# Performance work log

Measured on AMD Instinct MI355X. Metric: run time of the kernel, lower is better.

Reference implementation:

```python
import jax, jax.numpy as jnp
import numpy as np

N_NODES = 50000
N_EDGES = 1_000_000
D_IN = 64
HID = 64
N_GRAPHS = 128


def setup_inputs() -> dict:
    key = jax.random.key(0)
    ks = jax.random.split(key, 12)
    s = 1.0 / np.sqrt(HID)
    x = jax.random.normal(ks[0], (N_NODES, D_IN), dtype=jnp.float32)
    edge_index = jax.random.randint(ks[1], (2, N_EDGES), 0, N_NODES, dtype=jnp.int32)
    # every graph id occupied, sorted (like PyG batch vector)
    batch_index = (jnp.arange(N_NODES, dtype=jnp.int32) * N_GRAPHS) // N_NODES
    return {
        "x": x,
        "Wl0": jax.random.normal(ks[2], (HID, D_IN), jnp.float32) * s,
        "Wr0": jax.random.normal(ks[3], (HID, D_IN), jnp.float32) * s,
        "bl0": jax.random.normal(ks[4], (HID,), jnp.float32) * s,
        "Wl": jax.random.normal(ks[5], (HID, HID), jnp.float32) * s,
        "Wr": jax.random.normal(ks[6], (HID, HID), jnp.float32) * s,
        "bl": jax.random.normal(ks[7], (HID,), jnp.float32) * s,
        "W1": jax.random.normal(ks[8], (HID, HID), jnp.float32) * s,
        "b1": jax.random.normal(ks[9], (HID,), jnp.float32) * s,
        "W2": jax.random.normal(ks[10], (3, HID), jnp.float32) * s,
        "b2": jax.random.normal(ks[11], (3,), jnp.float32) * s,
        "edge_index": edge_index,
        "batch_index": batch_index,
    }


def _sage_conv(x, Wl, Wr, bl, src, dst, n_nodes):
    # PyG SAGEConv (aggr='mean'): out = lin_l(mean_{j in N(i)} x_j) + lin_r(x_i)
    msgs = jnp.take(x, src, axis=0)                               # [E, D] gather
    agg = jax.ops.segment_sum(msgs, dst, num_segments=n_nodes)    # [N, D] scatter-add
    deg = jax.ops.segment_sum(jnp.ones((src.shape[0],), x.dtype), dst, num_segments=n_nodes)
    mean = agg / jnp.clip(deg, 1.0)[:, None]
    return mean @ Wl.T + bl + x @ Wr.T


def reference(x, Wl0, Wr0, bl0, Wl, Wr, bl, W1, b1, W2, b2, edge_index, batch_index):
    src, dst = edge_index[0], edge_index[1]
    n = x.shape[0]
    h = jnp.tanh(_sage_conv(x, Wl0, Wr0, bl0, src, dst, n))
    # same SAGEConv instance reused 3 times
    for _ in range(3):
        h = jnp.tanh(_sage_conv(h, Wl, Wr, bl, src, dst, n))
    pooled = jax.ops.segment_max(h, batch_index, num_segments=N_GRAPHS)  # [G, H]
    # same lin1 reused 3 times
    g = pooled
    for _ in range(3):
        g = jnp.tanh(g @ W1.T + b1)
    return g @ W2.T + b2
```

## Files before the change

kernel.cpp:

```cpp
#include <hip/hip_runtime.h>
#include <math.h>

#define NT 256

typedef unsigned short ushort_t;
typedef unsigned int uint_t;

__device__ __forceinline__ float rlf(float v, int l) {
    return __int_as_float(__builtin_amdgcn_readlane(__float_as_int(v), l));
}
__device__ __forceinline__ int rli(int v, int l) {
    return __builtin_amdgcn_readlane(v, l);
}
__device__ __forceinline__ int imax(int a, int b) { return a > b ? a : b; }

__device__ __forceinline__ ushort_t f2bf_rne(float f) {
    uint_t u = __float_as_uint(f);
    uint_t r = u + 0x7FFF + ((u >> 16) & 1);
    return (ushort_t)(r >> 16);
}
__device__ __forceinline__ float bf2f(ushort_t b) {
    return __uint_as_float(((uint_t)b) << 16);
}


__global__ void zero_i32(int* __restrict__ p, int n) {
    int t = blockIdx.x * blockDim.x + threadIdx.x;
    if (t < n) p[t] = 0;
}

__global__ void hist_dst(int* __restrict__ cnt, const int* __restrict__ dst, int n_edges) {
    int e = blockIdx.x * blockDim.x + threadIdx.x;
    if (e < n_edges) atomicAdd(&cnt[dst[e]], 1);
}

__global__ void scan_blocks(const int* __restrict__ cnt, int* __restrict__ bsum, int n) {
    __shared__ int s[NT];
    int i = blockIdx.x * NT + threadIdx.x;
    s[threadIdx.x] = (i < n) ? cnt[i] : 0;
    __syncthreads();
    for (int off = NT / 2; off > 0; off >>= 1) {
        if (threadIdx.x < off) s[threadIdx.x] += s[threadIdx.x + off];
        __syncthreads();
    }
    if (threadIdx.x == 0) bsum[blockIdx.x] = s[0];
}

__global__ void scan_bsum(const int* __restrict__ bsum, int* __restrict__ boff,
                          int nb, int* __restrict__ row_off, int n) {
    __shared__ int s[1024];
    int tid = threadIdx.x;
    int v = (tid < nb) ? bsum[tid] : 0;
    s[tid] = v;
    __syncthreads();
    for (int off = 1; off < 1024; off <<= 1) {
        int t = (tid >= off) ? s[tid - off] : 0;
        __syncthreads();
        s[tid] += t;
        __syncthreads();
    }
    if (tid < nb) boff[tid] = s[tid] - v;
    if (tid == nb - 1) row_off[n] = s[tid];
}

__global__ void scan_final(const int* __restrict__ cnt, const int* __restrict__ boff,
                           int* __restrict__ row_off, int* __restrict__ cursor, int n) {
    __shared__ int s[NT];
    int i = blockIdx.x * NT + threadIdx.x;
    int v = (i < n) ? cnt[i] : 0;
    s[threadIdx.x] = v;
    __syncthreads();
    for (int off = 1; off < NT; off <<= 1) {
        int t = (threadIdx.x >= off) ? s[threadIdx.x - off] : 0;
        __syncthreads();
        s[threadIdx.x] += t;
        __syncthreads();
    }
    if (i < n) {
        int ex = boff[blockIdx.x] + s[threadIdx.x] - v;
        row_off[i] = ex;
        cursor[i] = ex;
    }
}

__global__ void edge_scatter(int* __restrict__ csr_src, int* __restrict__ cursor,
                             const int* __restrict__ src, const int* __restrict__ dst,
                             int n_edges) {
    int e = blockIdx.x * blockDim.x + threadIdx.x;
    if (e < n_edges) {
        int p = atomicAdd(&cursor[dst[e]], 1);
        csr_src[p] = src[e];
    }
}

__global__ void wtrans(float* __restrict__ out, const float* __restrict__ W) {
    int t = blockIdx.x * blockDim.x + threadIdx.x;
    if (t < 4096) {
        int kk = t & 3, f = (t >> 2) & 63, k4 = t >> 8;
        out[t] = W[f * 64 + k4 * 4 + kk];
    }
}

__global__ void f2bf_kern(ushort_t* __restrict__ o, const float* __restrict__ in, int n) {
    int t = blockIdx.x * blockDim.x + threadIdx.x;
    if (t < n) o[t] = f2bf_rne(in[t]);
}


__global__ void pool_init(float* __restrict__ pooled, int n) {
    int t = blockIdx.x * blockDim.x + threadIdx.x;
    if (t < n) pooled[t] = -INFINITY;
}

__device__ __forceinline__ void atomicMaxFloat(float* addr, float value) {
    if (value >= 0.0f)
        atomicMax((int*)addr, __float_as_int(value));
    else
        atomicMin((unsigned int*)addr, (unsigned int)__float_as_int(value));
}

__global__ __launch_bounds__(NT, 8) void sage_layer(
    float* __restrict__ out, ushort_t* __restrict__ out_bf,
    float* __restrict__ pooled,
    const float* __restrict__ h_in, const ushort_t* __restrict__ hb_in,
    const int* __restrict__ row_off, const int* __restrict__ csr_src,
    const int* __restrict__ batch,
    const float* __restrict__ Wl, const float* __restrict__ WrT,
    const float* __restrict__ bl,
    int n_nodes, int do_pool) {
    __shared__ float WL[4096];
    int tid = threadIdx.x;
    for (int t = tid; t < 4096; t += NT) {
        int kk = t & 3, f = (t >> 2) & 63, k4 = t >> 8;
        WL[t] = Wl[f * 64 + k4 * 4 + kk];
    }
    __syncthreads();

    int lane = tid & 63;
    int gwave = (blockIdx.x * NT + tid) >> 6;
    int nwaves = (gridDim.x * NT) >> 6;
    float bias = bl[lane];

    for (int q = gwave; q * 4 < n_nodes; q += nwaves) {
        int base = q * 4;
        float mean0 = 0.f, mean1 = 0.f, mean2 = 0.f, mean3 = 0.f;
        float hv0 = 0.f, hv1 = 0.f, hv2 = 0.f, hv3 = 0.f;

#define GATHER_NODE(MEAN, HV, N)                                              \
        {                                                                     \
            int i = base + (N);                                               \
            if (i < n_nodes) {                                                \
                int beg = row_off[i];                                         \
                int end_ = row_off[i + 1];                                    \
                int deg = end_ - beg;                                         \
                float a0 = 0.f, a1 = 0.f;                                     \
                for (int cb = beg; cb < end_; cb += 64) {                     \
                    int m = end_ - cb; if (m > 64) m = 64;                    \
                    int lidx = cb + (lane < m ? lane : m - 1);                \
                    int idx = csr_src[lidx];                                  \
                    for (int j = 0; j < m; j += 8) {                          \
                        int mm1 = m - 1;                                      \
                        int s0 = rli(idx, j);                                 \
                        int s1 = rli(idx, j + 1 < m ? j + 1 : mm1);           \
                        int s2 = rli(idx, j + 2 < m ? j + 2 : mm1);           \
                        int s3 = rli(idx, j + 3 < m ? j + 3 : mm1);           \
                        int s4 = rli(idx, j + 4 < m ? j + 4 : mm1);           \
                        int s5 = rli(idx, j + 5 < m ? j + 5 : mm1);           \
                        int s6 = rli(idx, j + 6 < m ? j + 6 : mm1);           \
                        int s7 = rli(idx, j + 7 < m ? j + 7 : mm1);           \
                        float v0 = bf2f(hb_in[(s0 << 6) + lane]);             \
                        float v1 = bf2f(hb_in[(s1 << 6) + lane]);             \
                        float v2 = bf2f(hb_in[(s2 << 6) + lane]);             \
                        float v3 = bf2f(hb_in[(s3 << 6) + lane]);             \
                        float v4 = bf2f(hb_in[(s4 << 6) + lane]);             \
                        float v5 = bf2f(hb_in[(s5 << 6) + lane]);             \
                        float v6 = bf2f(hb_in[(s6 << 6) + lane]);             \
                        float v7 = bf2f(hb_in[(s7 << 6) + lane]);             \
                        a0 += v0;                                             \
                        a1 += (j + 1 < m) ? v1 : 0.f;                         \
                        a0 += (j + 2 < m) ? v2 : 0.f;                         \
                        a1 += (j + 3 < m) ? v3 : 0.f;                         \
                        a0 += (j + 4 < m) ? v4 : 0.f;                         \
                        a1 += (j + 5 < m) ? v5 : 0.f;                         \
                        a0 += (j + 6 < m) ? v6 : 0.f;                         \
                        a1 += (j + 7 < m) ? v7 : 0.f;                         \
                    }                                                         \
                }                                                             \
                MEAN = (a0 + a1) * (1.0f / (float)(deg > 0 ? deg : 1));       \
                HV = h_in[(size_t)i * 64 + lane];                             \
            }                                                                 \
        }

        GATHER_NODE(mean0, hv0, 0)
        GATHER_NODE(mean1, hv1, 1)
        GATHER_NODE(mean2, hv2, 2)
        GATHER_NODE(mean3, hv3, 3)
#undef GATHER_NODE

        float o0 = bias, o1 = bias, o2 = bias, o3 = bias;
        for (int k4 = 0; k4 < 16; ++k4) {
            float4 wl = *(const float4*)&WL[k4 * 256 + lane * 4];
            float4 wr = *(const float4*)&WrT[k4 * 256 + lane * 4];
            int kb = k4 * 4;
#define DENSE_KK(WLK, WRK, KK)                                                \
            {                                                                 \
                int k = kb + (KK);                                            \
                o0 += rlf(mean0, k) * (WLK) + rlf(hv0, k) * (WRK);            \
                o1 += rlf(mean1, k) * (WLK) + rlf(hv1, k) * (WRK);            \
                o2 += rlf(mean2, k) * (WLK) + rlf(hv2, k) * (WRK);            \
                o3 += rlf(mean3, k) * (WLK) + rlf(hv3, k) * (WRK);            \
            }
            DENSE_KK(wl.x, wr.x, 0)
            DENSE_KK(wl.y, wr.y, 1)
            DENSE_KK(wl.z, wr.z, 2)
            DENSE_KK(wl.w, wr.w, 3)
#undef DENSE_KK
        }

        o0 = tanhf(o0); o1 = tanhf(o1); o2 = tanhf(o2); o3 = tanhf(o3);

#define WRITE_NODE(O, N)                                                      \
        {                                                                     \
            int i = base + (N);                                               \
            if (i < n_nodes) {                                                \
                if (do_pool) {                                                \
                    atomicMaxFloat(&pooled[(size_t)batch[i] * 64 + lane], O); \
                } else {                                                      \
                    out[(size_t)i * 64 + lane] = O;                           \
                    out_bf[(size_t)i * 64 + lane] = f2bf_rne(O);              \
                }                                                             \
            }                                                                 \
        }
        WRITE_NODE(o0, 0)
        WRITE_NODE(o1, 1)
        WRITE_NODE(o2, 2)
        WRITE_NODE(o3, 3)
#undef WRITE_NODE
    }
}

__global__ void head(float* __restrict__ out, const float* __restrict__ pooled,
                     const float* __restrict__ W1, const float* __restrict__ b1,
                     const float* __restrict__ W2, const float* __restrict__ b2) {
    __shared__ float W1T[64][64];
    int tid = threadIdx.x;
    for (int t = tid; t < 4096; t += NT) {
        int f = t >> 6, k = t & 63;
        W1T[k][f] = W1[t];
    }
    __syncthreads();

    int lane = tid & 63;
    int g = blockIdx.x * (NT >> 6) + (tid >> 6);
    float v = pooled[(size_t)g * 64 + lane];
    float bias = b1[lane];
#pragma unroll
    for (int it = 0; it < 3; ++it) {
        float acc = bias;
#pragma unroll
        for (int k = 0; k < 64; ++k) {
            acc += rlf(v, k) * W1T[k][lane];
        }
        v = tanhf(acc);
    }
#pragma unroll
    for (int j = 0; j < 3; ++j) {
        float p = v * W2[j * 64 + lane];
#pragma unroll
        for (int off = 32; off >= 1; off >>= 1) p += __shfl_xor(p, off);
        if (lane == 0) out[g * 3 + j] = p + b2[j];
    }
}


extern "C" void kernel_launch(void* const* d_in, const int* in_sizes, int n_in,
                              void* d_out, int out_size, void* d_ws, size_t ws_size,
                              hipStream_t stream) {
    const float* x   = (const float*)d_in[0];
    const float* Wl0 = (const float*)d_in[1];
    const float* Wr0 = (const float*)d_in[2];
    const float* bl0 = (const float*)d_in[3];
    const float* Wl  = (const float*)d_in[4];
    const float* Wr  = (const float*)d_in[5];
    const float* bl  = (const float*)d_in[6];
    const float* W1  = (const float*)d_in[7];
    const float* b1  = (const float*)d_in[8];
    const float* W2  = (const float*)d_in[9];
    const float* b2  = (const float*)d_in[10];
    const int* ei    = (const int*)d_in[11];
    const int* batch = (const int*)d_in[12];

    int n_nodes = in_sizes[0] / 64;
    int n_edges = in_sizes[11] / 2;
    const int* src = ei;
    const int* dst = ei + n_edges;

    int nb = (n_nodes + NT - 1) / NT;
    size_t nfeat = (size_t)n_nodes * 64;

    float* bufA   = (float*)d_ws;
    float* bufB   = bufA + nfeat;
    int* csr_src  = (int*)(bufB + nfeat);
    int* row_off  = csr_src + n_edges;
    int* cursor   = row_off + (n_nodes + 1);
    int* cnt      = cursor + n_nodes;
    int* bsum     = cnt + n_nodes;
    int* boff     = bsum + nb;
    float* pooled = (float*)(boff + nb);
    float* wr0t   = pooled + 128 * 64;
    float* wrt    = wr0t + 4096;
    ushort_t* bfA = (ushort_t*)(wrt + 4096);
    ushort_t* bfB = bfA + nfeat;

    int eblk = (n_edges + NT - 1) / NT;
    const int pers_blk = 2048;

    zero_i32<<<nb, NT, 0, stream>>>(cnt, n_nodes);
    hist_dst<<<eblk, NT, 0, stream>>>(cnt, dst, n_edges);
    scan_blocks<<<nb, NT, 0, stream>>>(cnt, bsum, n_nodes);
    scan_bsum<<<1, 1024, 0, stream>>>(bsum, boff, nb, row_off, n_nodes);
    scan_final<<<nb, NT, 0, stream>>>(cnt, boff, row_off, cursor, n_nodes);
    edge_scatter<<<eblk, NT, 0, stream>>>(csr_src, cursor, src, dst, n_edges);

    wtrans<<<16, NT, 0, stream>>>(wr0t, Wr0);
    wtrans<<<16, NT, 0, stream>>>(wrt, Wr);
    f2bf_kern<<<(int)((nfeat + NT - 1) / NT), NT, 0, stream>>>(bfA, x, (int)nfeat);
    pool_init<<<(128 * 64 + NT - 1) / NT, NT, 0, stream>>>(pooled, 128 * 64);

    sage_layer<<<pers_blk, NT, 0, stream>>>(bufA, bfB, pooled, x, bfA,
                                            row_off, csr_src, batch,
                                            Wl0, wr0t, bl0, n_nodes, 0);
    sage_layer<<<pers_blk, NT, 0, stream>>>(bufB, bfA, pooled, bufA, bfB,
                                            row_off, csr_src, batch,
                                            Wl, wrt, bl, n_nodes, 0);
    sage_layer<<<pers_blk, NT, 0, stream>>>(bufA, bfB, pooled, bufB, bfA,
                                            row_off, csr_src, batch,
                                            Wl, wrt, bl, n_nodes, 0);
    sage_layer<<<pers_blk, NT, 0, stream>>>(bufB, bfA, pooled, bufA, bfB,
                                            row_off, csr_src, batch,
                                            Wl, wrt, bl, n_nodes, 1);

    head<<<32, NT, 0, stream>>>((float*)d_out, pooled, W1, b1, W2, b2);
}
```

Measured before the change: 458.9 us.

## Compute SAGE dense transform with bf16 MFMA over shared-memory node tiles

```diff
diff --git a/kernel.cpp b/kernel.cpp
--- a/kernel.cpp
+++ b/kernel.cpp
@@ -5,10 +5,9 @@
 
 typedef unsigned short ushort_t;
 typedef unsigned int uint_t;
-
-__device__ __forceinline__ float rlf(float v, int l) {
-    return __int_as_float(__builtin_amdgcn_readlane(__float_as_int(v), l));
-}
+typedef __attribute__((ext_vector_type(8))) short bf16x8;
+typedef __attribute__((ext_vector_type(4))) float f32x4;
+
 __device__ __forceinline__ int rli(int v, int l) {
     return __builtin_amdgcn_readlane(v, l);
 }
@@ -21,6 +20,9 @@
 }
 __device__ __forceinline__ float bf2f(ushort_t b) {
     return __uint_as_float(((uint_t)b) << 16);
+}
+__device__ __forceinline__ float rlf(float v, int l) {
+    return __int_as_float(__builtin_amdgcn_readlane(__float_as_int(v), l));
 }
 
 
@@ -93,17 +95,25 @@
     }
 }
 
-__global__ void wtrans(float* __restrict__ out, const float* __restrict__ W) {
-    int t = blockIdx.x * blockDim.x + threadIdx.x;
-    if (t < 4096) {
-        int kk = t & 3, f = (t >> 2) & 63, k4 = t >> 8;
-        out[t] = W[f * 64 + k4 * 4 + kk];
-    }
-}
 
 __global__ void f2bf_kern(ushort_t* __restrict__ o, const float* __restrict__ in, int n) {
     int t = blockIdx.x * blockDim.x + threadIdx.x;
     if (t < n) o[t] = f2bf_rne(in[t]);
+}
+
+__global__ void pack_w(ushort_t* __restrict__ packed, const float* __restrict__ Wl,
+                       const float* __restrict__ Wr) {
+    int t = blockIdx.x * blockDim.x + threadIdx.x;
+    if (t < 8192) {
+        int i = t & 7;
+        int lane = (t >> 3) & 63;
+        int nt = (t >> 9) & 3;
+        int ks = t >> 11;
+        int k = ks * 32 + ((lane >> 4) << 3) + i;
+        int f = nt * 16 + (lane & 15);
+        float w = (k < 64) ? Wl[f * 64 + k] : Wr[f * 64 + (k - 64)];
+        packed[t] = f2bf_rne(w);
+    }
 }
 
 
@@ -120,122 +130,111 @@
 }
 
 __global__ __launch_bounds__(NT, 8) void sage_layer(
-    float* __restrict__ out, ushort_t* __restrict__ out_bf,
-    float* __restrict__ pooled,
-    const float* __restrict__ h_in, const ushort_t* __restrict__ hb_in,
+    ushort_t* __restrict__ out_bf, float* __restrict__ pooled,
+    const ushort_t* __restrict__ hb_in,
     const int* __restrict__ row_off, const int* __restrict__ csr_src,
     const int* __restrict__ batch,
-    const float* __restrict__ Wl, const float* __restrict__ WrT,
+    const ushort_t* __restrict__ pw,
     const float* __restrict__ bl,
     int n_nodes, int do_pool) {
-    __shared__ float WL[4096];
+    __shared__ ushort_t A[32 * 136];
     int tid = threadIdx.x;
-    for (int t = tid; t < 4096; t += NT) {
-        int kk = t & 3, f = (t >> 2) & 63, k4 = t >> 8;
-        WL[t] = Wl[f * 64 + k4 * 4 + kk];
-    }
-    __syncthreads();
-
     int lane = tid & 63;
-    int gwave = (blockIdx.x * NT + tid) >> 6;
-    int nwaves = (gridDim.x * NT) >> 6;
-    float bias = bl[lane];
-
-    for (int q = gwave; q * 4 < n_nodes; q += nwaves) {
-        int base = q * 4;
-        float mean0 = 0.f, mean1 = 0.f, mean2 = 0.f, mean3 = 0.f;
-        float hv0 = 0.f, hv1 = 0.f, hv2 = 0.f, hv3 = 0.f;
-
-#define GATHER_NODE(MEAN, HV, N)                                              \
-        {                                                                     \
-            int i = base + (N);                                               \
-            if (i < n_nodes) {                                                \
-                int beg = row_off[i];                                         \
-                int end_ = row_off[i + 1];                                    \
-                int deg = end_ - beg;                                         \
-                float a0 = 0.f, a1 = 0.f;                                     \
-                for (int cb = beg; cb < end_; cb += 64) {                     \
-                    int m = end_ - cb; if (m > 64) m = 64;                    \
-                    int lidx = cb + (lane < m ? lane : m - 1);                \
-                    int idx = csr_src[lidx];                                  \
-                    for (int j = 0; j < m; j += 8) {                          \
-                        int mm1 = m - 1;                                      \
-                        int s0 = rli(idx, j);                                 \
-                        int s1 = rli(idx, j + 1 < m ? j + 1 : mm1);           \
-                        int s2 = rli(idx, j + 2 < m ? j + 2 : mm1);           \
-                        int s3 = rli(idx, j + 3 < m ? j + 3 : mm1);           \
-                        int s4 = rli(idx, j + 4 < m ? j + 4 : mm1);           \
-                        int s5 = rli(idx, j + 5 < m ? j + 5 : mm1);           \
-                        int s6 = rli(idx, j + 6 < m ? j + 6 : mm1);           \
-                        int s7 = rli(idx, j + 7 < m ? j + 7 : mm1);           \
-                        float v0 = bf2f(hb_in[(s0 << 6) + lane]);             \
-                        float v1 = bf2f(hb_in[(s1 << 6) + lane]);             \
-                        float v2 = bf2f(hb_in[(s2 << 6) + lane]);             \
-                        float v3 = bf2f(hb_in[(s3 << 6) + lane]);             \
-                        float v4 = bf2f(hb_in[(s4 << 6) + lane]);             \
-                        float v5 = bf2f(hb_in[(s5 << 6) + lane]);             \
-                        float v6 = bf2f(hb_in[(s6 << 6) + lane]);             \
-                        float v7 = bf2f(hb_in[(s7 << 6) + lane]);             \
-                        a0 += v0;                                             \
-                        a1 += (j + 1 < m) ? v1 : 0.f;                         \
-                        a0 += (j + 2 < m) ? v2 : 0.f;                         \
-                        a1 += (j + 3 < m) ? v3 : 0.f;                         \
-                        a0 += (j + 4 < m) ? v4 : 0.f;                         \
-                        a1 += (j + 5 < m) ? v5 : 0.f;                         \
-                        a0 += (j + 6 < m) ? v6 : 0.f;                         \
-                        a1 += (j + 7 < m) ? v7 : 0.f;                         \
-                    }                                                         \
-                }                                                             \
-                MEAN = (a0 + a1) * (1.0f / (float)(deg > 0 ? deg : 1));       \
-                HV = h_in[(size_t)i * 64 + lane];                             \
-            }                                                                 \
+    int v = tid >> 6;
+    int g0 = blockIdx.x * 32 + v * 8;
+
+    int roidx = g0 + (lane < 9 ? lane : 8);
+    if (roidx > n_nodes) roidx = n_nodes;
+    int ro = row_off[roidx];
+
+#pragma unroll
+    for (int n = 0; n < 8; ++n) {
+        int g = g0 + n;
+        int row = v * 8 + n;
+        if (g < n_nodes) {
+            int b = rli(ro, n);
+            int e_ = rli(ro, n + 1);
+            int d = e_ - b;
+            float mean = 0.f;
+            if (d <= 64) {
+                int idx = csr_src[b + (lane < d ? lane : imax(d - 1, 0))];
+                float a0 = 0.f, a1 = 0.f;
+                for (int j = 0; j < d; j += 8) {
+                    int mm1 = d - 1;
+                    int s0 = rli(idx, j);
+                    int s1 = rli(idx, j + 1 < d ? j + 1 : mm1);
+                    int s2 = rli(idx, j + 2 < d ? j + 2 : mm1);
+                    int s3 = rli(idx, j + 3 < d ? j + 3 : mm1);
+                    int s4 = rli(idx, j + 4 < d ? j + 4 : mm1);
+                    int s5 = rli(idx, j + 5 < d ? j + 5 : mm1);
+                    int s6 = rli(idx, j + 6 < d ? j + 6 : mm1);
+                    int s7 = rli(idx, j + 7 < d ? j + 7 : mm1);
+                    float v0 = bf2f(hb_in[(s0 << 6) + lane]);
+                    float v1 = bf2f(hb_in[(s1 << 6) + lane]);
+                    float v2 = bf2f(hb_in[(s2 << 6) + lane]);
+                    float v3 = bf2f(hb_in[(s3 << 6) + lane]);
+                    float v4 = bf2f(hb_in[(s4 << 6) + lane]);
+                    float v5 = bf2f(hb_in[(s5 << 6) + lane]);
+                    float v6 = bf2f(hb_in[(s6 << 6) + lane]);
+                    float v7 = bf2f(hb_in[(s7 << 6) + lane]);
+                    a0 += v0;
+                    a1 += (j + 1 < d) ? v1 : 0.f;
+                    a0 += (j + 2 < d) ? v2 : 0.f;
+                    a1 += (j + 3 < d) ? v3 : 0.f;
+                    a0 += (j + 4 < d) ? v4 : 0.f;
+                    a1 += (j + 5 < d) ? v5 : 0.f;
+                    a0 += (j + 6 < d) ? v6 : 0.f;
+                    a1 += (j + 7 < d) ? v7 : 0.f;
+                }
+                mean = (a0 + a1) * (1.0f / (float)imax(d, 1));
+            } else {
+                float aa = 0.f;
+                for (int cb = b; cb < e_; cb += 64) {
+                    int m = e_ - cb; if (m > 64) m = 64;
+                    int lidx = cb + (lane < m ? lane : m - 1);
+                    int idx = csr_src[lidx];
+                    for (int j = 0; j < m; ++j)
+                        aa += bf2f(hb_in[(rli(idx, j) << 6) + lane]);
+                }
+                mean = aa * (1.0f / (float)imax(d, 1));
+            }
+            A[row * 136 + lane] = f2bf_rne(mean);
+            A[row * 136 + 64 + lane] = hb_in[(size_t)g * 64 + lane];
+        } else {
+            A[row * 136 + lane] = 0;
+            A[row * 136 + 64 + lane] = 0;
         }
-
-        GATHER_NODE(mean0, hv0, 0)
-        GATHER_NODE(mean1, hv1, 1)
-        GATHER_NODE(mean2, hv2, 2)
-        GATHER_NODE(mean3, hv3, 3)
-#undef GATHER_NODE
-
-        float o0 = bias, o1 = bias, o2 = bias, o3 = bias;
-        for (int k4 = 0; k4 < 16; ++k4) {
-            float4 wl = *(const float4*)&WL[k4 * 256 + lane * 4];
-            float4 wr = *(const float4*)&WrT[k4 * 256 + lane * 4];
-            int kb = k4 * 4;
-#define DENSE_KK(WLK, WRK, KK)                                                \
-            {                                                                 \
-                int k = kb + (KK);                                            \
-                o0 += rlf(mean0, k) * (WLK) + rlf(hv0, k) * (WRK);            \
-                o1 += rlf(mean1, k) * (WLK) + rlf(hv1, k) * (WRK);            \
-                o2 += rlf(mean2, k) * (WLK) + rlf(hv2, k) * (WRK);            \
-                o3 += rlf(mean3, k) * (WLK) + rlf(hv3, k) * (WRK);            \
+    }
+    __syncthreads();
+
+    int rowtile = v >> 1;
+    int a_row = rowtile * 16 + (lane & 15);
+    int kbase = (lane >> 4) << 3;
+#pragma unroll
+    for (int p = 0; p < 2; ++p) {
+        int nt = (v & 1) * 2 + p;
+        f32x4 acc = {0.f, 0.f, 0.f, 0.f};
+#pragma unroll
+        for (int ks = 0; ks < 4; ++ks) {
+            bf16x8 af = *reinterpret_cast<const bf16x8*>(&A[a_row * 136 + ks * 32 + kbase]);
+            bf16x8 bf = *reinterpret_cast<const bf16x8*>(&pw[(((ks << 2) + nt) * 64 + lane) << 3]);
+            acc = __builtin_amdgcn_mfma_f32_16x16x32_bf16(af, bf, acc, 0, 0, 0);
+        }
+        int c = nt * 16 + (lane & 15);
+        float bias = bl[c];
+        int rbase = blockIdx.x * 32 + rowtile * 16 + ((lane >> 4) << 2);
+#pragma unroll
+        for (int j = 0; j < 4; ++j) {
+            int g = rbase + j;
+            if (g < n_nodes) {
+                float o = tanhf(acc[j] + bias);
+                if (do_pool) {
+                    atomicMaxFloat(&pooled[(size_t)batch[g] * 64 + c], o);
+                } else {
+                    out_bf[(size_t)g * 64 + c] = f2bf_rne(o);
+                }
             }
-            DENSE_KK(wl.x, wr.x, 0)
-            DENSE_KK(wl.y, wr.y, 1)
-            DENSE_KK(wl.z, wr.z, 2)
-            DENSE_KK(wl.w, wr.w, 3)
-#undef DENSE_KK
         }
-
-        o0 = tanhf(o0); o1 = tanhf(o1); o2 = tanhf(o2); o3 = tanhf(o3);
-
-#define WRITE_NODE(O, N)                                                      \
-        {                                                                     \
-            int i = base + (N);                                               \
-            if (i < n_nodes) {                                                \
-                if (do_pool) {                                                \
-                    atomicMaxFloat(&pooled[(size_t)batch[i] * 64 + lane], O); \
-                } else {                                                      \
-                    out[(size_t)i * 64 + lane] = O;                           \
-                    out_bf[(size_t)i * 64 + lane] = f2bf_rne(O);              \
-                }                                                             \
-            }                                                                 \
-        }
-        WRITE_NODE(o0, 0)
-        WRITE_NODE(o1, 1)
-        WRITE_NODE(o2, 2)
-        WRITE_NODE(o3, 3)
-#undef WRITE_NODE
     }
 }
 
@@ -298,22 +297,21 @@
     int nb = (n_nodes + NT - 1) / NT;
     size_t nfeat = (size_t)n_nodes * 64;
 
-    float* bufA   = (float*)d_ws;
-    float* bufB   = bufA + nfeat;
-    int* csr_src  = (int*)(bufB + nfeat);
+    int* csr_src  = (int*)d_ws;
     int* row_off  = csr_src + n_edges;
     int* cursor   = row_off + (n_nodes + 1);
     int* cnt      = cursor + n_nodes;
     int* bsum     = cnt + n_nodes;
     int* boff     = bsum + nb;
     float* pooled = (float*)(boff + nb);
-    float* wr0t   = pooled + 128 * 64;
-    float* wrt    = wr0t + 4096;
-    ushort_t* bfA = (ushort_t*)(wrt + 4096);
+    ushort_t* pw0 = (ushort_t*)(pooled + 128 * 64);
+    ushort_t* pw  = pw0 + 8192;
+    ushort_t* bfX = pw + 8192;
+    ushort_t* bfA = bfX + nfeat;
     ushort_t* bfB = bfA + nfeat;
 
     int eblk = (n_edges + NT - 1) / NT;
-    const int pers_blk = 2048;
+    int sage_blk = (n_nodes + 31) / 32;
 
     zero_i32<<<nb, NT, 0, stream>>>(cnt, n_nodes);
     hist_dst<<<eblk, NT, 0, stream>>>(cnt, dst, n_edges);
@@ -322,23 +320,19 @@
     scan_final<<<nb, NT, 0, stream>>>(cnt, boff, row_off, cursor, n_nodes);
     edge_scatter<<<eblk, NT, 0, stream>>>(csr_src, cursor, src, dst, n_edges);
 
-    wtrans<<<16, NT, 0, stream>>>(wr0t, Wr0);
-    wtrans<<<16, NT, 0, stream>>>(wrt, Wr);
-    f2bf_kern<<<(int)((nfeat + NT - 1) / NT), NT, 0, stream>>>(bfA, x, (int)nfeat);
+    f2bf_kern<<<(int)((nfeat + NT - 1) / NT), NT, 0, stream>>>(bfX, x, (int)nfeat);
+    pack_w<<<32, NT, 0, stream>>>(pw0, Wl0, Wr0);
+    pack_w<<<32, NT, 0, stream>>>(pw, Wl, Wr);
     pool_init<<<(128 * 64 + NT - 1) / NT, NT, 0, stream>>>(pooled, 128 * 64);
 
-    sage_layer<<<pers_blk, NT, 0, stream>>>(bufA, bfB, pooled, x, bfA,
-                                            row_off, csr_src, batch,
-                                            Wl0, wr0t, bl0, n_nodes, 0);
-    sage_layer<<<pers_blk, NT, 0, stream>>>(bufB, bfA, pooled, bufA, bfB,
-                                            row_off, csr_src, batch,
-                                            Wl, wrt, bl, n_nodes, 0);
-    sage_layer<<<pers_blk, NT, 0, stream>>>(bufA, bfB, pooled, bufB, bfA,
-                                            row_off, csr_src, batch,
-                                            Wl, wrt, bl, n_nodes, 0);
-    sage_layer<<<pers_blk, NT, 0, stream>>>(bufB, bfA, pooled, bufA, bfB,
-                                            row_off, csr_src, batch,
-                                            Wl, wrt, bl, n_nodes, 1);
+    sage_layer<<<sage_blk, NT, 0, stream>>>(bfA, pooled, bfX, row_off, csr_src,
+                                            batch, pw0, bl0, n_nodes, 0);
+    sage_layer<<<sage_blk, NT, 0, stream>>>(bfB, pooled, bfA, row_off, csr_src,
+                                            batch, pw, bl, n_nodes, 0);
+    sage_layer<<<sage_blk, NT, 0, stream>>>(bfA, pooled, bfB, row_off, csr_src,
+                                            batch, pw, bl, n_nodes, 0);
+    sage_layer<<<sage_blk, NT, 0, stream>>>(bfB, pooled, bfA, row_off, csr_src,
+                                            batch, pw, bl, n_nodes, 1);
 
     head<<<32, NT, 0, stream>>>((float*)d_out, pooled, W1, b1, W2, b2);
 }
```

Result: faster. 396.6 us (-13.6%).
